# Kernel tuning notes

Measured on AMD Instinct MI355X. Metric: run time of the kernel, lower is better.

## Reference

```python
import jax, jax.numpy as jnp
import numpy as np

BS, F, C, H, W = 2, 8, 64, 128, 128
HEADS = 4

def build_edges(bs, f):
    rows, cols, ec = [], [], 0
    for b in range(bs):
        s = b * (2 * f + 2)
        v = list(range(s, s + f)); d = list(range(s + f, s + 2 * f))
        t = s + 2 * f; g = t + 1
        for grp in (v, d, v + d, v + d, v + d + [t], [t], [g]):
            rows += grp; cols += [ec] * len(grp); ec += 1
    return np.asarray(rows, np.int32), np.asarray(cols, np.int32), ec

ROW, COL, NUM_EDGES = build_edges(BS, F)

def conv2d_s2(x, w, b):  # Conv2d k3 s2 p1 + ReLU
    y = jax.lax.conv_general_dilated(x, w, (2, 2), [(1, 1), (1, 1)],
        dimension_numbers=('NCHW', 'OIHW', 'NCHW'))
    return jax.nn.relu(y + b[None, :, None, None])

def conv_t2(x, w, b):  # ConvTranspose2d k3 s2 p1 op1 + ReLU; w: (in,out,3,3)
    wt = jnp.flip(w, (2, 3)).transpose(1, 0, 2, 3)
    y = jax.lax.conv_general_dilated(x, wt, (1, 1), [(1, 2), (1, 2)],
        lhs_dilation=(2, 2), dimension_numbers=('NCHW', 'OIHW', 'NCHW'))
    return jax.nn.relu(y + b[None, :, None, None])

def layer_norm(x, eps=1e-5):  # affine params are default ones/zeros
    mu = x.mean(-1, keepdims=True)
    var = ((x - mu) ** 2).mean(-1, keepdims=True)
    return (x - mu) / jnp.sqrt(var + eps)

def group_norm(x, groups=32, eps=1e-5):
    n, c = x.shape
    xg = x.reshape(n, groups, c // groups)
    mu = xg.mean(-1, keepdims=True)
    var = ((xg - mu) ** 2).mean(-1, keepdims=True)
    return ((xg - mu) / jnp.sqrt(var + eps)).reshape(n, c)

def se_layer(x, w1, w2):  # squeeze over node dim 0
    y = jax.nn.sigmoid(jax.nn.relu(x.mean(0) @ w1.T) @ w2.T)
    return x * y

def hypergraph_conv(x, lin_w, att, edge_w, edge_attr, out_ch):
    # PyG HypergraphConv, use_attention=True, attention_mode='node', heads=4,
    # concat=False, bias=False, eval mode (dropout inactive)
    n = x.shape[0]
    xl = (x @ lin_w.T).reshape(n, HEADS, out_ch)
    ea = (edge_attr @ lin_w.T).reshape(-1, HEADS, out_ch)
    a = (jnp.concatenate([xl[ROW], ea[COL]], axis=-1) * att).sum(-1)  # (E, heads)
    a = jax.nn.leaky_relu(a, 0.2)
    a = jnp.exp(a - jax.ops.segment_max(a, COL, num_segments=NUM_EDGES)[COL])
    a = a / (jax.ops.segment_sum(a, COL, num_segments=NUM_EDGES)[COL] + 1e-16)
    D = jax.ops.segment_sum(edge_w[COL], ROW, num_segments=n)
    D = jnp.where(D > 0, 1.0 / D, 0.0)
    B = jax.ops.segment_sum(jnp.ones(ROW.shape[0], x.dtype), COL, num_segments=NUM_EDGES)
    B = jnp.where(B > 0, 1.0 / B, 0.0)
    e = jax.ops.segment_sum(B[COL][:, None, None] * a[:, :, None] * xl[ROW], COL, num_segments=NUM_EDGES)
    o = jax.ops.segment_sum(D[ROW][:, None, None] * a[:, :, None] * e[COL], ROW, num_segments=n)
    return o.mean(1)  # concat=False -> head mean

def setup_inputs() -> dict:
    key = jax.random.key(0)
    ks = jax.random.split(key, 32)
    def n(k, shape, s=1.0):
        return jax.random.normal(k, shape, jnp.float32) * s
    def u(k, shape):
        return jax.random.uniform(k, shape, jnp.float32)
    return {
        'vision_feat': n(ks[0], (BS, F, C, H, W)), 'vision_pos': n(ks[1], (BS, F, C, H, W), 0.1),
        'motion_feat': n(ks[2], (BS, F, C, H, W)), 'motion_pos': n(ks[3], (BS, F, C, H, W), 0.1),
        'text_feat': n(ks[4], (BS, C, 16)), 'text_pos': n(ks[5], (BS, C, 16), 0.1),
        'cv1_w': n(ks[6], (2 * C, C, 3, 3), 0.04), 'cv1_b': n(ks[7], (2 * C,), 0.01),
        'cv2_w': n(ks[8], (4 * C, 2 * C, 3, 3), 0.03), 'cv2_b': n(ks[9], (4 * C,), 0.01),
        'dc1_w': n(ks[10], (2 * C, C, 3, 3), 0.04), 'dc1_b': n(ks[11], (2 * C,), 0.01),
        'dc2_w': n(ks[12], (4 * C, 2 * C, 3, 3), 0.03), 'dc2_b': n(ks[13], (4 * C,), 0.01),
        'tc1_w': n(ks[14], (4 * C, 2 * C, 3, 3), 0.03), 'tc1_b': n(ks[15], (2 * C,), 0.01),
        'tc2_w': n(ks[16], (2 * C, C, 3, 3), 0.04), 'tc2_b': n(ks[17], (C,), 0.01),
        'lin1_w': n(ks[18], (HEADS * 8 * C, 4 * C), 0.06), 'att1': n(ks[19], (1, HEADS, 16 * C), 0.05),
        'lin2_w': n(ks[20], (HEADS * 4 * C, 8 * C), 0.04), 'att2': n(ks[21], (1, HEADS, 8 * C), 0.05),
        'ew1': u(ks[22], (2 * F * BS + 2,)), 'ew2': u(ks[23], (2 * F * BS + 2,)),
        'ea1': u(ks[24], (2 * F * BS + 2, 4 * C)), 'ea2': u(ks[25], (2 * F * BS + 2, 8 * C)),
        'se1_w1': n(ks[26], (8 * C // 16, 8 * C), 0.06), 'se1_w2': n(ks[27], (8 * C, 8 * C // 16), 0.15),
        'se2_w1': n(ks[28], (4 * C // 16, 4 * C), 0.08), 'se2_w2': n(ks[29], (4 * C, 4 * C // 16), 0.2),
    }

def reference(vision_feat, vision_pos, motion_feat, motion_pos, text_feat, text_pos,
              cv1_w, cv1_b, cv2_w, cv2_b, dc1_w, dc1_b, dc2_w, dc2_b,
              tc1_w, tc1_b, tc2_w, tc2_b, lin1_w, att1, lin2_w, att2,
              ew1, ew2, ea1, ea2, se1_w1, se1_w2, se2_w1, se2_w2):
    bs, f, c, h, w = vision_feat.shape
    # text_pool: AdaptiveMaxPool1d(4) on L=16 -> exact windows of 4; view(bs,-1)
    tn = (text_feat + text_pos).reshape(bs, c, 4, 4).max(-1).reshape(bs, 4 * c)
    v0 = (vision_feat + vision_pos).reshape(bs * f, c, h, w)
    v1 = conv2d_s2(v0, cv1_w, cv1_b)          # (bs*f, 2c, h/2, w/2)
    v2 = conv2d_s2(v1, cv2_w, cv2_b)          # (bs*f, 4c, h/4, w/4)
    vn = layer_norm(v2.max((2, 3)))           # AdaptiveMaxPool2d(1) + LayerNorm
    d0 = (motion_feat + motion_pos).reshape(bs * f, c, h, w)
    dn = layer_norm(conv2d_s2(conv2d_s2(d0, dc1_w, dc1_b), dc2_w, dc2_b).max((2, 3)))
    vb = vn.reshape(bs, f, 4 * c); db = dn.reshape(bs, f, 4 * c)
    obs = tn + (vb + db).mean(1)              # observer = mean(text+v+d) over frames
    x = jnp.concatenate([vb, db, tn[:, None], obs[:, None]], axis=1).reshape(bs * (2 * f + 2), 4 * c)
    x = se_layer(group_norm(jax.nn.relu(hypergraph_conv(x, lin1_w, att1, ew1, ea1, 8 * c))), se1_w1, se1_w2)
    x = se_layer(group_norm(jax.nn.relu(hypergraph_conv(x, lin2_w, att2, ew2, ea2, 4 * c))), se2_w1, se2_w2)
    xb = x.reshape(bs, 2 * f + 2, 4 * c)
    # obs_pool: AdaptiveMaxPool1d(c) on L=4c -> windows of 4
    observers = (tn + xb[:, -1]).reshape(bs, c, 4).max(-1)
    vg = xb[:, :f].reshape(bs * f, 4 * c)
    # bilinear upsample of 1x1 == broadcast; transconv doubles size so the
    # subsequent F.interpolate calls to (h/2,w/2) and (h,w) are identities
    vr = v2 + vg[:, :, None, None]
    vr = v1 + conv_t2(vr, tc1_w, tc1_b)
    vr = v0 + conv_t2(vr, tc2_w, tc2_b)
    return vr, observers
```

## Files before the change

### kernel.cpp

```cpp
#include <hip/hip_runtime.h>
#include <hip/hip_bf16.h>
#include <cstddef>
#include <cstdint>

#define DEV_INLINE __device__ __forceinline__
#define AS1 __attribute__((address_space(1)))
#define AS3 __attribute__((address_space(3)))

typedef __attribute__((ext_vector_type(8))) short short8;
typedef __attribute__((ext_vector_type(4))) float f32x4;
typedef __attribute__((ext_vector_type(2))) float f32x2;
typedef __attribute__((ext_vector_type(4))) unsigned short us4;

DEV_INLINE unsigned short f2bf(float f) {
  uint32_t u = __builtin_bit_cast(uint32_t, f);
  uint32_t r = (u + 0x7fffu + ((u >> 16) & 1u)) >> 16;
  return (unsigned short)r;
}
DEV_INLINE float bf2f(unsigned short u) {
  return __builtin_bit_cast(float, (uint32_t)u << 16);
}

DEV_INLINE void gl_lds16(const float* g, float* l) {
  __builtin_amdgcn_global_load_lds((AS1 void*)const_cast<float*>(g),
                                   (AS3 void*)l, 16, 0, 0);
}

__device__ __constant__ int c_cs[15] = {0,8,16,32,48,65,66,67,75,83,99,115,132,133,134};
__device__ __constant__ int c_row[134] = {
  0,1,2,3,4,5,6,7,
  8,9,10,11,12,13,14,15,
  0,1,2,3,4,5,6,7,8,9,10,11,12,13,14,15,
  0,1,2,3,4,5,6,7,8,9,10,11,12,13,14,15,
  0,1,2,3,4,5,6,7,8,9,10,11,12,13,14,15,16,
  16,
  17,
  18,19,20,21,22,23,24,25,
  26,27,28,29,30,31,32,33,
  18,19,20,21,22,23,24,25,26,27,28,29,30,31,32,33,
  18,19,20,21,22,23,24,25,26,27,28,29,30,31,32,33,
  18,19,20,21,22,23,24,25,26,27,28,29,30,31,32,33,34,
  34,
  35
};
__device__ __constant__ int c_col[134] = {
  0,0,0,0,0,0,0,0,
  1,1,1,1,1,1,1,1,
  2,2,2,2,2,2,2,2,2,2,2,2,2,2,2,2,
  3,3,3,3,3,3,3,3,3,3,3,3,3,3,3,3,
  4,4,4,4,4,4,4,4,4,4,4,4,4,4,4,4,4,
  5,
  6,
  7,7,7,7,7,7,7,7,
  8,8,8,8,8,8,8,8,
  9,9,9,9,9,9,9,9,9,9,9,9,9,9,9,9,
  10,10,10,10,10,10,10,10,10,10,10,10,10,10,10,10,
  11,11,11,11,11,11,11,11,11,11,11,11,11,11,11,11,11,
  12,
  13
};

__global__ __launch_bounds__(256) void k_prep(const float* __restrict__ a,
                                              const float* __restrict__ b,
                                              unsigned short* __restrict__ o) {
  __shared__ float sa[16 * 260];
  __shared__ float sb[16 * 260];
  int bid = blockIdx.x;
  int xb = bid & 1, y = (bid >> 1) & 127, n = bid >> 8;
  int t = threadIdx.x;
  int w = t >> 6, lane = t & 63;
  int ciq = lane >> 4;
  int xo = (lane & 15) * 4;
  const size_t base = ((size_t)n * 64) * 16384 + (size_t)y * 128 + xb * 64;
#pragma unroll
  for (int k = 0; k < 4; ++k) {
    int row = w * 16 + k * 4;
    const float* ga = a + base + (size_t)(row + ciq) * 16384 + xo;
    const float* gb = b + base + (size_t)(row + ciq) * 16384 + xo;
    gl_lds16(ga, &sa[(4 * w + k) * 260]);
    gl_lds16(gb, &sb[(4 * w + k) * 260]);
  }
  __syncthreads();
  auto rd = [](const float* s, int ci, int x) {
    return s[(ci >> 2) * 260 + (ci & 3) * 64 + x];
  };
  unsigned int* op = (unsigned int*)(o + (((size_t)n * 128 + y) * 128 + xb * 64) * 64);
#pragma unroll
  for (int it = 0; it < 2; ++it) {
    int i = t + it * 256;
    int x = i >> 3, cq = i & 7;
    uint4 v;
    unsigned int vv[4];
#pragma unroll
    for (int j = 0; j < 4; ++j) {
      int c2 = cq * 8 + j * 2;
      unsigned int lo = f2bf(rd(sa, c2, x) + rd(sb, c2, x));
      unsigned int hi = f2bf(rd(sa, c2 + 1, x) + rd(sb, c2 + 1, x));
      vv[j] = lo | (hi << 16);
    }
    v.x = vv[0]; v.y = vv[1]; v.z = vv[2]; v.w = vv[3];
    *reinterpret_cast<uint4*>(op + x * 32 + cq * 4) = v;
  }
}

__global__ void k_wtrans_all(const float* __restrict__ cv1w, const float* __restrict__ dc1w,
                             const float* __restrict__ cv2w, const float* __restrict__ dc2w,
                             const float* __restrict__ tc1w, const float* __restrict__ tc2w,
                             unsigned short* __restrict__ wtb) {
  int idx = blockIdx.x * 256 + threadIdx.x;
  const float* src; int off, lci, lco; bool tra;
  if (idx < 73728)        { src = cv1w; off = 0;       lci = 6; lco = 7; tra = false; }
  else if (idx < 147456)  { src = dc1w; off = 73728;   lci = 6; lco = 7; tra = false; }
  else if (idx < 442368)  { src = cv2w; off = 147456;  lci = 7; lco = 8; tra = false; }
  else if (idx < 737280)  { src = dc2w; off = 442368;  lci = 7; lco = 8; tra = false; }
  else if (idx < 1032192) { src = tc1w; off = 737280;  lci = 8; lco = 7; tra = true;  }
  else if (idx < 1105920) { src = tc2w; off = 1032192; lci = 7; lco = 6; tra = true;  }
  else return;
  int l = idx - off;
  int ci = l & ((1 << lci) - 1);
  int r = l >> lci;
  int co = r & ((1 << lco) - 1);
  int tap = r >> lco;
  size_t si = tra ? (((size_t)ci << lco) + co) * 9 + tap
                  : (((size_t)co << lci) + ci) * 9 + tap;
  wtb[idx] = f2bf(src[si]);
}

template<int CI, int CO, int HO, int WO, int ROUT>
__global__ __launch_bounds__(512, 3) void k_conv_mfma(
    const unsigned short* __restrict__ in,
    const unsigned short* __restrict__ wT,
    const float* __restrict__ bias,
    unsigned short* __restrict__ outn) {
  constexpr int HIN = HO * 2, WIN = WO * 2;
  constexpr int XHP = WO + 2;
  constexpr int R = 2 * ROUT + 1;
  constexpr int NPOS = R * 2 * XHP;
  constexpr int NCH = NPOS * 4;
  constexpr int NCS = CI / 32;
  constexpr int KIT = (NCH + 511) / 512;
  constexpr int CB = CO / 128;
  constexpr int OB = HO / ROUT;
  __shared__ short8 sIn[NPOS * 5];
  int bid = blockIdx.x;
  int cb = bid % CB; bid /= CB;
  int oyb = bid % OB; int n = bid / OB;
  int tid = threadIdx.x;
  int wid = tid >> 6, lane = tid & 63;
  int wm = wid >> 1, wn = wid & 1;
  int llo = lane & 15, lhi = lane >> 4;
  f32x4 acc[2][2] = {};
  const int iy0 = oyb * (2 * ROUT) - 1;
  short8 rv[KIT];
  auto loadr = [&](int cs) {
#pragma unroll
    for (int k = 0; k < KIT; ++k) {
      int i = tid + k * 512;
      short8 v = {};
      if (i < NCH) {
        int c = i & 3, q = i >> 2;
        int xh = q % XHP; int q2 = q / XHP;
        int p = q2 & 1, l = q2 >> 1;
        int x = 2 * xh + p - 1;
        int iy = iy0 + l;
        if (x >= 0 && x < WIN && iy >= 0 && iy < HIN)
          v = *reinterpret_cast<const short8*>(in + ((((size_t)n * HIN + iy) * WIN + x) * CI + cs * 32 + c * 8));
      }
      rv[k] = v;
    }
  };
  auto writes = [&]() {
#pragma unroll
    for (int k = 0; k < KIT; ++k) {
      int i = tid + k * 512;
      if (i < NCH) sIn[(i >> 2) * 5 + (i & 3)] = rv[k];
    }
  };
  loadr(0);
  for (int cs = 0; cs < NCS; ++cs) {
    writes();
    __syncthreads();
    if (cs + 1 < NCS) loadr(cs + 1);
    short8 afr9[9][2];
#pragma unroll
    for (int tap = 0; tap < 9; ++tap)
#pragma unroll
      for (int m = 0; m < 2; ++m) {
        int co = cb * 128 + wm * 32 + m * 16 + llo;
        afr9[tap][m] = *reinterpret_cast<const short8*>(wT + (((size_t)tap * CO + co) * CI + cs * 32 + lhi * 8));
      }
#pragma unroll
    for (int tap = 0; tap < 9; ++tap) {
      const int ky = tap / 3, kx = tap % 3;
      short8 bfr[2];
#pragma unroll
      for (int n2 = 0; n2 < 2; ++n2) {
        int pix = wn * 32 + n2 * 16 + llo;
        int oyl = (ROUT == 2) ? (pix >> 5) : 0;
        int ox = pix - oyl * WO;
        int lrow = 2 * oyl + ky;
        int pos = (lrow * 2 + (kx & 1)) * XHP + ox + (kx >> 1);
        bfr[n2] = sIn[pos * 5 + lhi];
      }
#pragma unroll
      for (int m = 0; m < 2; ++m)
#pragma unroll
        for (int n2 = 0; n2 < 2; ++n2)
          acc[m][n2] = __builtin_amdgcn_mfma_f32_16x16x32_bf16(afr9[tap][m], bfr[n2], acc[m][n2], 0, 0, 0);
    }
    __syncthreads();
  }
#pragma unroll
  for (int m = 0; m < 2; ++m) {
    int co0 = cb * 128 + wm * 32 + m * 16 + lhi * 4;
    f32x4 bv = *reinterpret_cast<const f32x4*>(bias + co0);
#pragma unroll
    for (int n2 = 0; n2 < 2; ++n2) {
      int pix = wn * 32 + n2 * 16 + llo;
      int oyl = (ROUT == 2) ? (pix >> 5) : 0;
      int ox = pix - oyl * WO;
      int oy = oyb * ROUT + oyl;
      us4 pk;
      pk[0] = f2bf(fmaxf(acc[m][n2][0] + bv[0], 0.f));
      pk[1] = f2bf(fmaxf(acc[m][n2][1] + bv[1], 0.f));
      pk[2] = f2bf(fmaxf(acc[m][n2][2] + bv[2], 0.f));
      pk[3] = f2bf(fmaxf(acc[m][n2][3] + bv[3], 0.f));
      *reinterpret_cast<us4*>(outn + ((((size_t)n * HO + oy) * WO + ox) * CO + co0)) = pk;
    }
  }
}

template<int CI, int CO, int Hi, int Wi, int QR, bool OBF, bool GADD>
__global__ __launch_bounds__(256, 3) void k_deconv_mfma(
    const unsigned short* __restrict__ in,
    const unsigned short* __restrict__ wT,
    const float* __restrict__ bias,
    const unsigned short* __restrict__ resn,
    const float* __restrict__ gsrc,
    unsigned short* __restrict__ outn,
    float* __restrict__ outc) {
  constexpr int QC = 64 / QR;
  constexpr int WP = Wi + 1;
  constexpr int NPOS = (QR + 1) * WP;
  constexpr int NCH = NPOS * 4;
  constexpr int NCS = CI / 32;
  constexpr int KIT = (NCH + 255) / 256;
  constexpr int CB = CO / 64;
  constexpr int OB = Hi / QR;
  constexpr int Ho = Hi * 2, Wo = Wi * 2;
  __shared__ short8 sIn[NPOS * 5];
  int bid = blockIdx.x;
  int cb = bid % CB; bid /= CB;
  int oyb = bid % OB; int n = bid / OB;
  int tid = threadIdx.x;
  int wid = tid >> 6, lane = tid & 63;
  int wm = wid >> 1, wn = wid & 1;
  int llo = lane & 15, lhi = lane >> 4;
  int qy0 = oyb * QR;
  const float* g = nullptr;
  if constexpr (GADD) g = gsrc + ((size_t)((n >> 3) * 18 + (n & 7))) * 256;
  f32x4 acc[4][2][2] = {};
  constexpr int tap_p[9] = {3,2,3,1,0,1,3,2,3};
  constexpr int tap_b[9] = {3,2,2,1,0,0,1,0,0};
  short8 rv[KIT];
  auto loadr = [&](int cs) {
#pragma unroll
    for (int k = 0; k < KIT; ++k) {
      int i = tid + k * 256;
      short8 v = {};
      if (i < NCH) {
        int c = i & 3, q = i >> 2;
        int x = q % WP, l = q / WP;
        int iy = qy0 + l;
        if (x < Wi && iy < Hi) {
          v = *reinterpret_cast<const short8*>(in + (((size_t)(n * Hi + iy) * Wi + x) * CI + cs * 32 + c * 8));
          if constexpr (GADD) {
#pragma unroll
            for (int j = 0; j < 8; ++j) {
              float fv = bf2f((unsigned short)v[j]) + g[cs * 32 + c * 8 + j];
              v[j] = (short)f2bf(fv);
            }
          }
        }
      }
      rv[k] = v;
    }
  };
  auto writes = [&]() {
#pragma unroll
    for (int k = 0; k < KIT; ++k) {
      int i = tid + k * 256;
      if (i < NCH) sIn[(i >> 2) * 5 + (i & 3)] = rv[k];
    }
  };
  loadr(0);
  for (int cs = 0; cs < NCS; ++cs) {
    writes();
    __syncthreads();
    if (cs + 1 < NCS) loadr(cs + 1);
    short8 bfr[2][4];
#pragma unroll
    for (int n2 = 0; n2 < 2; ++n2) {
      int pix = wn * 32 + n2 * 16 + llo;
      int qyl = pix / QC, qx = pix % QC;
#pragma unroll
      for (int bs = 0; bs < 4; ++bs) {
        int pos = (qyl + (bs >> 1)) * WP + qx + (bs & 1);
        bfr[n2][bs] = sIn[pos * 5 + lhi];
      }
    }
#pragma unroll
    for (int m = 0; m < 2; ++m) {
      short8 afr9[9];
#pragma unroll
      for (int tap = 0; tap < 9; ++tap) {
        int co = cb * 64 + wm * 32 + m * 16 + llo;
        afr9[tap] = *reinterpret_cast<const short8*>(wT + (((size_t)tap * CO + co) * CI + cs * 32 + lhi * 8));
      }
#pragma unroll
      for (int tap = 0; tap < 9; ++tap)
#pragma unroll
        for (int n2 = 0; n2 < 2; ++n2)
          acc[tap_p[tap]][m][n2] = __builtin_amdgcn_mfma_f32_16x16x32_bf16(
              afr9[tap], bfr[n2][tap_b[tap]], acc[tap_p[tap]][m][n2], 0, 0, 0);
    }
    __syncthreads();
  }
#pragma unroll
  for (int m = 0; m < 2; ++m) {
    int co0 = cb * 64 + wm * 32 + m * 16 + lhi * 4;
    f32x4 bv = *reinterpret_cast<const f32x4*>(bias + co0);
#pragma unroll
    for (int n2 = 0; n2 < 2; ++n2) {
      int pix = wn * 32 + n2 * 16 + llo;
      int qyl = pix / QC, qx = pix % QC;
      int qy = qy0 + qyl;
      if constexpr (OBF) {
#pragma unroll
        for (int p = 0; p < 4; ++p) {
          int oy = 2 * qy + (p >> 1);
          int ox = 2 * qx + (p & 1);
          size_t ad = ((size_t)(n * Ho + oy) * Wo + ox) * CO + co0;
          us4 r = *reinterpret_cast<const us4*>(resn + ad);
          us4 pk;
#pragma unroll
          for (int c = 0; c < 4; ++c)
            pk[c] = f2bf(bf2f(r[c]) + fmaxf(acc[p][m][n2][c] + bv[c], 0.f));
          *reinterpret_cast<us4*>(outn + ad) = pk;
        }
      } else {
        int qx2 = 2 * qx;
#pragma unroll
        for (int dy = 0; dy < 2; ++dy) {
          int oy = 2 * qy + dy;
          size_t rb = ((size_t)(n * Ho + oy) * Wo + qx2) * CO + co0;
          us4 r0 = *reinterpret_cast<const us4*>(resn + rb);
          us4 r1 = *reinterpret_cast<const us4*>(resn + rb + CO);
#pragma unroll
          for (int c = 0; c < 4; ++c) {
            f32x2 st;
            st[0] = bf2f(r0[c]) + fmaxf(acc[dy * 2][m][n2][c] + bv[c], 0.f);
            st[1] = bf2f(r1[c]) + fmaxf(acc[dy * 2 + 1][m][n2][c] + bv[c], 0.f);
            __builtin_nontemporal_store(st,
                reinterpret_cast<f32x2*>(outc + ((size_t)(n * CO + co0 + c) * Ho + oy) * Wo + qx2));
          }
        }
      }
    }
  }
}

__global__ __launch_bounds__(256) void k_max_part(const unsigned short* __restrict__ x,
                                                  float* __restrict__ pmax) {
  int n = blockIdx.x >> 3, pg = blockIdx.x & 7;
  int t = threadIdx.x;
  int c8 = t & 31;
  int ps = t >> 5;
  const unsigned short* base = x + (size_t)n * 262144 + (size_t)pg * 32768 + (size_t)c8 * 8;
  float m[8];
#pragma unroll
  for (int j = 0; j < 8; ++j) m[j] = -1e30f;
  for (int p = ps * 16; p < ps * 16 + 16; ++p) {
    short8 v = *reinterpret_cast<const short8*>(base + (size_t)p * 256);
#pragma unroll
    for (int j = 0; j < 8; ++j) m[j] = fmaxf(m[j], bf2f((unsigned short)v[j]));
  }
  __shared__ float sred[8][264];
#pragma unroll
  for (int j = 0; j < 8; ++j) sred[ps][c8 * 8 + j] = m[j];
  __syncthreads();
  float mm = sred[0][t];
#pragma unroll
  for (int g = 1; g < 8; ++g) mm = fmaxf(mm, sred[g][t]);
  pmax[((size_t)n * 8 + pg) * 256 + t] = mm;
}

__global__ __launch_bounds__(256) void k_ln(const float* __restrict__ pmax,
                                            float* __restrict__ out) {
  int n = blockIdx.x, ch = threadIdx.x;
  float m = -1e30f;
#pragma unroll
  for (int g = 0; g < 8; ++g)
    m = fmaxf(m, pmax[((size_t)n * 8 + g) * 256 + ch]);
  __shared__ float r1[256], r2[256];
  r1[ch] = m; __syncthreads();
  for (int s = 128; s > 0; s >>= 1) { if (ch < s) r1[ch] += r1[ch + s]; __syncthreads(); }
  float mu = r1[0] * (1.f / 256.f);
  float d = m - mu;
  r2[ch] = d * d; __syncthreads();
  for (int s = 128; s > 0; s >>= 1) { if (ch < s) r2[ch] += r2[ch + s]; __syncthreads(); }
  out[(size_t)n * 256 + ch] = d * rsqrtf(r2[0] * (1.f / 256.f) + 1e-5f);
}

__global__ void k_build_x(const float* __restrict__ tf, const float* __restrict__ tp,
                          const float* __restrict__ vn, const float* __restrict__ dn,
                          float* __restrict__ tn, float* __restrict__ x0) {
  int b = blockIdx.x, ch = threadIdx.x;
  int c4 = ch >> 2, j = ch & 3;
  const float* p = tf + ((size_t)b * 64 + c4) * 16 + j * 4;
  const float* q = tp + ((size_t)b * 64 + c4) * 16 + j * 4;
  float tv = p[0] + q[0];
  tv = fmaxf(tv, p[1] + q[1]);
  tv = fmaxf(tv, p[2] + q[2]);
  tv = fmaxf(tv, p[3] + q[3]);
  tn[(size_t)b * 256 + ch] = tv;
  float s = 0.f;
  for (int f = 0; f < 8; ++f) {
    float vv = vn[((size_t)b * 8 + f) * 256 + ch];
    float dd = dn[((size_t)b * 8 + f) * 256 + ch];
    s += vv + dd;
    x0[((size_t)b * 18 + f) * 256 + ch] = vv;
    x0[((size_t)b * 18 + 8 + f) * 256 + ch] = dd;
  }
  x0[((size_t)b * 18 + 16) * 256 + ch] = tv;
  x0[((size_t)b * 18 + 17) * 256 + ch] = tv + s * (1.f / 8.f);
}

__global__ __launch_bounds__(256) void k_gnn_lin(
    const float* __restrict__ x, const float* __restrict__ ea,
    const float* __restrict__ w, float* __restrict__ y, int K, int M) {
  int chunks = M >> 8;
  int r = blockIdx.x / chunks;
  int ob = (blockIdx.x % chunks) * 256 + threadIdx.x;
  const float* src = (r < 36) ? (x + (size_t)r * K) : (ea + (size_t)(r - 36) * K);
  __shared__ __align__(16) float sxr[512];
  for (int k = threadIdx.x; k < K; k += 256) sxr[k] = src[k];
  __syncthreads();
  const float4* w4 = reinterpret_cast<const float4*>(w + (size_t)ob * K);
  const float4* x4 = reinterpret_cast<const float4*>(sxr);
  float acc = 0.f;
  int k4 = K >> 2;
  for (int k = 0; k < k4; ++k) {
    float4 a = x4[k], b = w4[k];
    acc += a.x * b.x + a.y * b.y + a.z * b.z + a.w * b.w;
  }
  y[(size_t)r * M + ob] = acc;
}

template<int OC>
__global__ __launch_bounds__(256) void k_gnn_attsm(
    const float* __restrict__ y, const float* __restrict__ att,
    float* __restrict__ attw) {
  int t = threadIdx.x;
  __shared__ float sx_s[144], seb_s[60];
  __shared__ float a_s[536];
  if (t < 200) {
    int r = t >> 2, h = t & 3;
    const float4* row = reinterpret_cast<const float4*>(y + ((size_t)r * 4 + h) * OC);
    const float4* ar = reinterpret_cast<const float4*>(att + (size_t)h * 2 * OC + (r < 36 ? 0 : OC));
    float s = 0.f;
#pragma unroll 4
    for (int k = 0; k < OC / 4; ++k) {
      float4 a = row[k], b = ar[k];
      s += a.x * b.x + a.y * b.y + a.z * b.z + a.w * b.w;
    }
    if (r < 36) sx_s[r * 4 + h] = s; else seb_s[(r - 36) * 4 + h] = s;
  }
  __syncthreads();
  for (int idx = t; idx < 536; idx += 256) {
    int i = idx >> 2, h = idx & 3;
    float v = sx_s[c_row[i] * 4 + h] + seb_s[c_col[i] * 4 + h];
    a_s[idx] = (v > 0.f) ? v : 0.2f * v;
  }
  __syncthreads();
  if (t < 56) {
    int c = t >> 2, h = t & 3;
    int st = c_cs[c], en = c_cs[c + 1];
    float m = -1e30f;
    for (int i = st; i < en; ++i) m = fmaxf(m, a_s[i * 4 + h]);
    float s = 0.f;
    for (int i = st; i < en; ++i) { float e = __expf(a_s[i * 4 + h] - m); a_s[i * 4 + h] = e; s += e; }
    float inv = 1.f / (s + 1e-16f);
    for (int i = st; i < en; ++i) a_s[i * 4 + h] *= inv;
  }
  __syncthreads();
  for (int idx = t; idx < 536; idx += 256) attw[idx] = a_s[idx];
}

template<int OC>
__global__ __launch_bounds__(256) void k_edge_agg(
    const float* __restrict__ y, const float* __restrict__ attw,
    float* __restrict__ eb) {
  int idx = blockIdx.x * 256 + threadIdx.x;
  if (idx >= 14 * 4 * OC) return;
  int ch = idx % OC;
  int h = (idx / OC) & 3;
  int c = idx / (4 * OC);
  int st = c_cs[c], en = c_cs[c + 1];
  float s = 0.f;
  for (int i = st; i < en; ++i)
    s += attw[i * 4 + h] * y[(size_t)c_row[i] * (4 * OC) + h * OC + ch];
  eb[idx] = s * (1.f / (float)(en - st));
}

template<int OC>
__global__ __launch_bounds__(256) void k_node_agg(
    const float* __restrict__ attw, const float* __restrict__ eb,
    const float* __restrict__ ew, float* __restrict__ ho) {
  int idx = blockIdx.x * 256 + threadIdx.x;
  if (idx >= 36 * OC) return;
  int ch = idx % OC;
  int node = idx / OC;
  int b = node / 18, ln = node % 18;
  int ncols, cols[4], gis[4];
  if (ln < 16) {
    ncols = 4;
    cols[0] = b * 7 + (ln < 8 ? 0 : 1); gis[0] = b * 67 + ln;
    cols[1] = b * 7 + 2; gis[1] = b * 67 + 16 + ln;
    cols[2] = b * 7 + 3; gis[2] = b * 67 + 32 + ln;
    cols[3] = b * 7 + 4; gis[3] = b * 67 + 48 + ln;
  } else if (ln == 16) {
    ncols = 2;
    cols[0] = b * 7 + 4; gis[0] = b * 67 + 64;
    cols[1] = b * 7 + 5; gis[1] = b * 67 + 65;
    cols[2] = cols[3] = 0; gis[2] = gis[3] = 0;
  } else {
    ncols = 1;
    cols[0] = b * 7 + 6; gis[0] = b * 67 + 66;
    cols[1] = cols[2] = cols[3] = 0; gis[1] = gis[2] = gis[3] = 0;
  }
  float dsum = 0.f;
#pragma unroll
  for (int k = 0; k < 4; ++k) if (k < ncols) dsum += ew[cols[k]];
  float D = dsum > 0.f ? 1.f / dsum : 0.f;
  float s = 0.f;
#pragma unroll
  for (int k = 0; k < 4; ++k) {
    if (k < ncols) {
#pragma unroll
      for (int h = 0; h < 4; ++h)
        s += attw[gis[k] * 4 + h] * eb[((size_t)cols[k] * 4 + h) * OC + ch];
    }
  }
  ho[idx] = fmaxf(0.25f * D * s, 0.f);
}

template<int C, int Cr>
__global__ __launch_bounds__(512) void k_gn_se(
    const float* __restrict__ hin, const float* __restrict__ w1,
    const float* __restrict__ w2, float* __restrict__ x) {
  int t = threadIdx.x;
  constexpr int gs = C >> 5;
  for (int idx = t; idx < 36 * 32; idx += 512) {
    int node = idx >> 5, g = idx & 31;
    const float* p = hin + (size_t)node * C + g * gs;
    float s = 0.f, s2 = 0.f;
#pragma unroll
    for (int k = 0; k < gs; ++k) { float v = p[k]; s += v; s2 += v * v; }
    float mu = s * (1.f / gs);
    float var = s2 * (1.f / gs) - mu * mu;
    float inv = rsqrtf(fmaxf(var, 0.f) + 1e-5f);
    float* q = x + (size_t)node * C + g * gs;
#pragma unroll
    for (int k = 0; k < gs; ++k) q[k] = (p[k] - mu) * inv;
  }
  __threadfence_block();
  __syncthreads();
  __shared__ float smean[C];
  __shared__ float spart[Cr][17];
  __shared__ float shid[Cr];
  __shared__ float sscale[C];
  if (t < C) {
    float s = 0.f;
    for (int nn = 0; nn < 36; ++nn) s += x[(size_t)nn * C + t];
    smean[t] = s * (1.f / 36.f);
  }
  __syncthreads();
  if (t < Cr * 16) {
    int hid = t >> 4, sub = t & 15;
    constexpr int CH = C / 16;
    float s = 0.f;
#pragma unroll
    for (int k = 0; k < CH; ++k)
      s += w1[(size_t)hid * C + sub * CH + k] * smean[sub * CH + k];
    spart[hid][sub] = s;
  }
  __syncthreads();
  if (t < Cr) {
    float s = 0.f;
#pragma unroll
    for (int k = 0; k < 16; ++k) s += spart[t][k];
    shid[t] = fmaxf(s, 0.f);
  }
  __syncthreads();
  if (t < C) {
    float s = 0.f;
#pragma unroll
    for (int k = 0; k < Cr; ++k) s += w2[(size_t)t * Cr + k] * shid[k];
    sscale[t] = 1.f / (1.f + __expf(-s));
  }
  __syncthreads();
  for (int idx = t; idx < 36 * C; idx += 512) x[idx] *= sscale[idx % C];
}

__global__ void k_obs(const float* __restrict__ tn, const float* __restrict__ x2,
                      float* __restrict__ out) {
  int t = threadIdx.x;
  if (t >= 128) return;
  int b = t >> 6, ch = t & 63;
  const float* a = tn + (size_t)b * 256 + ch * 4;
  const float* c = x2 + ((size_t)b * 18 + 17) * 256 + ch * 4;
  float m = a[0] + c[0];
  m = fmaxf(m, a[1] + c[1]);
  m = fmaxf(m, a[2] + c[2]);
  m = fmaxf(m, a[3] + c[3]);
  out[b * 64 + ch] = m;
}

extern "C" void kernel_launch(void* const* d_in, const int* in_sizes, int n_in,
                              void* d_out, int out_size, void* d_ws, size_t ws_size,
                              hipStream_t stream) {
  (void)in_sizes; (void)n_in; (void)out_size; (void)ws_size;
  const float* vf    = (const float*)d_in[0];
  const float* vp    = (const float*)d_in[1];
  const float* mf    = (const float*)d_in[2];
  const float* mp    = (const float*)d_in[3];
  const float* tf    = (const float*)d_in[4];
  const float* tp    = (const float*)d_in[5];
  const float* cv1w  = (const float*)d_in[6];
  const float* cv1b  = (const float*)d_in[7];
  const float* cv2w  = (const float*)d_in[8];
  const float* cv2b  = (const float*)d_in[9];
  const float* dc1w  = (const float*)d_in[10];
  const float* dc1b  = (const float*)d_in[11];
  const float* dc2w  = (const float*)d_in[12];
  const float* dc2b  = (const float*)d_in[13];
  const float* tc1w  = (const float*)d_in[14];
  const float* tc1b  = (const float*)d_in[15];
  const float* tc2w  = (const float*)d_in[16];
  const float* tc2b  = (const float*)d_in[17];
  const float* lin1w = (const float*)d_in[18];
  const float* att1  = (const float*)d_in[19];
  const float* lin2w = (const float*)d_in[20];
  const float* att2  = (const float*)d_in[21];
  const float* ew1   = (const float*)d_in[22];
  const float* ew2   = (const float*)d_in[23];
  const float* ea1   = (const float*)d_in[24];
  const float* ea2   = (const float*)d_in[25];
  const float* se1w1 = (const float*)d_in[26];
  const float* se1w2 = (const float*)d_in[27];
  const float* se2w1 = (const float*)d_in[28];
  const float* se2w2 = (const float*)d_in[29];

  float* ws  = (float*)d_ws;
  float* out = (float*)d_out;

  unsigned short* p0n = (unsigned short*)(ws);
  unsigned short* q1n = (unsigned short*)(ws + 8388608);
  unsigned short* t1n = (unsigned short*)(ws + 12582912);
  unsigned short* v2n = (unsigned short*)(ws + 16777216);
  unsigned short* wtb = (unsigned short*)(ws + 18874368);
  float* sm   = ws + 19427328;
  float* tn   = sm;
  float* vn   = sm + 512;
  float* dn   = sm + 4608;
  float* x0   = sm + 8704;
  float* xl   = sm + 17920;
  float* eb   = sm + 120520;
  float* ho   = sm + 149192;
  float* x1   = sm + 167624;
  float* x2   = sm + 186056;
  float* attw = sm + 195272;
  float* pmax = sm + 195904;

  unsigned short* wTc1 = wtb;
  unsigned short* wTd1 = wtb + 73728;
  unsigned short* wTc2 = wtb + 147456;
  unsigned short* wTd2 = wtb + 442368;
  unsigned short* wTt1 = wtb + 737280;
  unsigned short* wTt2 = wtb + 1032192;

  k_wtrans_all<<<4320, 256, 0, stream>>>(cv1w, dc1w, cv2w, dc2w, tc1w, tc2w, wtb);

  k_prep<<<4096, 256, 0, stream>>>(mf, mp, p0n);
  k_conv_mfma<64, 128, 64, 64, 1><<<1024, 512, 0, stream>>>(p0n, wTd1, dc1b, q1n);
  k_conv_mfma<128, 256, 32, 32, 2><<<512, 512, 0, stream>>>(q1n, wTd2, dc2b, v2n);
  k_max_part<<<128, 256, 0, stream>>>(v2n, pmax);
  k_ln<<<16, 256, 0, stream>>>(pmax, dn);

  k_prep<<<4096, 256, 0, stream>>>(vf, vp, p0n);
  k_conv_mfma<64, 128, 64, 64, 1><<<1024, 512, 0, stream>>>(p0n, wTc1, cv1b, q1n);
  k_conv_mfma<128, 256, 32, 32, 2><<<512, 512, 0, stream>>>(q1n, wTc2, cv2b, v2n);
  k_max_part<<<128, 256, 0, stream>>>(v2n, pmax);
  k_ln<<<16, 256, 0, stream>>>(pmax, vn);

  k_build_x<<<2, 256, 0, stream>>>(tf, tp, vn, dn, tn, x0);

  k_gnn_lin<<<50 * 8, 256, 0, stream>>>(x0, ea1, lin1w, xl, 256, 2048);
  k_gnn_attsm<512><<<1, 256, 0, stream>>>(xl, att1, attw);
  k_edge_agg<512><<<112, 256, 0, stream>>>(xl, attw, eb);
  k_node_agg<512><<<72, 256, 0, stream>>>(attw, eb, ew1, ho);
  k_gn_se<512, 32><<<1, 512, 0, stream>>>(ho, se1w1, se1w2, x1);

  k_gnn_lin<<<50 * 4, 256, 0, stream>>>(x1, ea2, lin2w, xl, 512, 1024);
  k_gnn_attsm<256><<<1, 256, 0, stream>>>(xl, att2, attw);
  k_edge_agg<256><<<56, 256, 0, stream>>>(xl, attw, eb);
  k_node_agg<256><<<36, 256, 0, stream>>>(attw, eb, ew2, ho);
  k_gn_se<256, 16><<<1, 512, 0, stream>>>(ho, se2w1, se2w2, x2);

  k_obs<<<1, 128, 0, stream>>>(tn, x2, out + 16777216);

  k_deconv_mfma<256, 128, 32, 32, 2, true, true><<<512, 256, 0, stream>>>(
      v2n, wTt1, tc1b, q1n, x2, t1n, nullptr);
  k_deconv_mfma<128, 64, 64, 64, 1, false, false><<<1024, 256, 0, stream>>>(
      t1n, wTt2, tc2b, p0n, nullptr, nullptr, out);
}
```

Before: 480.6 us.

## Batch motion and visual encoder branches into single conv launches

The motion and visual conv encoder branches were run back to back, each with its own launches. They now run in shared launches: the conv kernels pick input, weights and bias per block from the batch index, and max-pool and layer norm run once over both branches. This doubles the grid of each launch to fill the GPU better and halves the launch count. k_prep is also reshaped to 512 threads per full row, reusing one LDS buffer for both input tensors. Workspace layout changes, and the output buffer is used as scratch for intermediates.

```diff
diff --git a/kernel.cpp b/kernel.cpp
--- a/kernel.cpp
+++ b/kernel.cpp
@@ -60,43 +60,53 @@
   13
 };
 
-__global__ __launch_bounds__(256) void k_prep(const float* __restrict__ a,
+__global__ __launch_bounds__(512) void k_prep(const float* __restrict__ a,
                                               const float* __restrict__ b,
                                               unsigned short* __restrict__ o) {
-  __shared__ float sa[16 * 260];
-  __shared__ float sb[16 * 260];
+  __shared__ float sbuf[32 * 260];
   int bid = blockIdx.x;
-  int xb = bid & 1, y = (bid >> 1) & 127, n = bid >> 8;
+  int y = bid & 127, n = bid >> 7;
   int t = threadIdx.x;
   int w = t >> 6, lane = t & 63;
-  int ciq = lane >> 4;
-  int xo = (lane & 15) * 4;
-  const size_t base = ((size_t)n * 64) * 16384 + (size_t)y * 128 + xb * 64;
+  int cio = lane >> 5;
+  int xg4 = (lane & 31) * 4;
+  const size_t base = ((size_t)n * 64) * 16384 + (size_t)y * 128;
 #pragma unroll
   for (int k = 0; k < 4; ++k) {
-    int row = w * 16 + k * 4;
-    const float* ga = a + base + (size_t)(row + ciq) * 16384 + xo;
-    const float* gb = b + base + (size_t)(row + ciq) * 16384 + xo;
-    gl_lds16(ga, &sa[(4 * w + k) * 260]);
-    gl_lds16(gb, &sb[(4 * w + k) * 260]);
-  }
-  __syncthreads();
-  auto rd = [](const float* s, int ci, int x) {
-    return s[(ci >> 2) * 260 + (ci & 3) * 64 + x];
+    int c = w * 4 + k;
+    gl_lds16(a + base + (size_t)(2 * c + cio) * 16384 + xg4, &sbuf[c * 260]);
+  }
+  __syncthreads();
+  auto rd = [&](int ci, int x) {
+    return sbuf[(ci >> 1) * 260 + (ci & 1) * 128 + x];
   };
-  unsigned int* op = (unsigned int*)(o + (((size_t)n * 128 + y) * 128 + xb * 64) * 64);
+  float av[2][8];
 #pragma unroll
   for (int it = 0; it < 2; ++it) {
-    int i = t + it * 256;
+    int i = t + it * 512;
+    int x = i >> 3, cq = i & 7;
+#pragma unroll
+    for (int j = 0; j < 8; ++j) av[it][j] = rd(cq * 8 + j, x);
+  }
+  __syncthreads();
+#pragma unroll
+  for (int k = 0; k < 4; ++k) {
+    int c = w * 4 + k;
+    gl_lds16(b + base + (size_t)(2 * c + cio) * 16384 + xg4, &sbuf[c * 260]);
+  }
+  __syncthreads();
+  unsigned int* op = (unsigned int*)(o + (((size_t)n * 128 + y) * 128) * 64);
+#pragma unroll
+  for (int it = 0; it < 2; ++it) {
+    int i = t + it * 512;
     int x = i >> 3, cq = i & 7;
     uint4 v;
     unsigned int vv[4];
 #pragma unroll
-    for (int j = 0; j < 4; ++j) {
-      int c2 = cq * 8 + j * 2;
-      unsigned int lo = f2bf(rd(sa, c2, x) + rd(sb, c2, x));
-      unsigned int hi = f2bf(rd(sa, c2 + 1, x) + rd(sb, c2 + 1, x));
-      vv[j] = lo | (hi << 16);
+    for (int jj = 0; jj < 4; ++jj) {
+      unsigned int lo = f2bf(av[it][2 * jj]     + rd(cq * 8 + 2 * jj, x));
+      unsigned int hi = f2bf(av[it][2 * jj + 1] + rd(cq * 8 + 2 * jj + 1, x));
+      vv[jj] = lo | (hi << 16);
     }
     v.x = vv[0]; v.y = vv[1]; v.z = vv[2]; v.w = vv[3];
     *reinterpret_cast<uint4*>(op + x * 32 + cq * 4) = v;
@@ -126,11 +136,11 @@
   wtb[idx] = f2bf(src[si]);
 }
 
-template<int CI, int CO, int HO, int WO, int ROUT>
-__global__ __launch_bounds__(512, 3) void k_conv_mfma(
-    const unsigned short* __restrict__ in,
-    const unsigned short* __restrict__ wT,
-    const float* __restrict__ bias,
+template<int CI, int CO, int HO, int WO, int ROUT, bool SPLIT_IN>
+__global__ __launch_bounds__(512, 3) void k_conv_mfma_b(
+    const unsigned short* __restrict__ in0, const unsigned short* __restrict__ in1,
+    const unsigned short* __restrict__ wT0, const unsigned short* __restrict__ wT1,
+    const float* __restrict__ b0, const float* __restrict__ b1,
     unsigned short* __restrict__ outn) {
   constexpr int HIN = HO * 2, WIN = WO * 2;
   constexpr int XHP = WO + 2;
@@ -145,6 +155,11 @@
   int bid = blockIdx.x;
   int cb = bid % CB; bid /= CB;
   int oyb = bid % OB; int n = bid / OB;
+  int br = n >> 4;
+  const unsigned short* in = SPLIT_IN ? (br ? in1 : in0) : in0;
+  const unsigned short* wT = br ? wT1 : wT0;
+  const float* bias = br ? b1 : b0;
+  int ni = SPLIT_IN ? (n & 15) : n;
   int tid = threadIdx.x;
   int wid = tid >> 6, lane = tid & 63;
   int wm = wid >> 1, wn = wid & 1;
@@ -164,7 +179,7 @@
         int x = 2 * xh + p - 1;
         int iy = iy0 + l;
         if (x >= 0 && x < WIN && iy >= 0 && iy < HIN)
-          v = *reinterpret_cast<const short8*>(in + ((((size_t)n * HIN + iy) * WIN + x) * CI + cs * 32 + c * 8));
+          v = *reinterpret_cast<const short8*>(in + ((((size_t)ni * HIN + iy) * WIN + x) * CI + cs * 32 + c * 8));
       }
       rv[k] = v;
     }
@@ -413,7 +428,7 @@
 }
 
 __global__ void k_build_x(const float* __restrict__ tf, const float* __restrict__ tp,
-                          const float* __restrict__ vn, const float* __restrict__ dn,
+                          const float* __restrict__ nb,
                           float* __restrict__ tn, float* __restrict__ x0) {
   int b = blockIdx.x, ch = threadIdx.x;
   int c4 = ch >> 2, j = ch & 3;
@@ -424,6 +439,8 @@
   tv = fmaxf(tv, p[2] + q[2]);
   tv = fmaxf(tv, p[3] + q[3]);
   tn[(size_t)b * 256 + ch] = tv;
+  const float* dn = nb;
+  const float* vn = nb + 16 * 256;
   float s = 0.f;
   for (int f = 0; f < 8; ++f) {
     float vv = vn[((size_t)b * 8 + f) * 256 + ch];
@@ -665,15 +682,13 @@
   float* ws  = (float*)d_ws;
   float* out = (float*)d_out;
 
-  unsigned short* p0n = (unsigned short*)(ws);
-  unsigned short* q1n = (unsigned short*)(ws + 8388608);
-  unsigned short* t1n = (unsigned short*)(ws + 12582912);
-  unsigned short* v2n = (unsigned short*)(ws + 16777216);
-  unsigned short* wtb = (unsigned short*)(ws + 18874368);
-  float* sm   = ws + 19427328;
+  unsigned short* p0nm = (unsigned short*)(ws);
+  unsigned short* p0nv = (unsigned short*)(ws + 8388608);
+  unsigned short* q1nb = (unsigned short*)(ws + 16777216);
+  unsigned short* wtb  = (unsigned short*)(ws + 25165824);
+  float* sm   = ws + 25718784;
   float* tn   = sm;
-  float* vn   = sm + 512;
-  float* dn   = sm + 4608;
+  float* nb   = sm + 512;
   float* x0   = sm + 8704;
   float* xl   = sm + 17920;
   float* eb   = sm + 120520;
@@ -683,6 +698,9 @@
   float* attw = sm + 195272;
   float* pmax = sm + 195904;
 
+  unsigned short* v2nb = (unsigned short*)d_out;
+  unsigned short* t1n = (unsigned short*)(ws);
+
   unsigned short* wTc1 = wtb;
   unsigned short* wTd1 = wtb + 73728;
   unsigned short* wTc2 = wtb + 147456;
@@ -692,19 +710,17 @@
 
   k_wtrans_all<<<4320, 256, 0, stream>>>(cv1w, dc1w, cv2w, dc2w, tc1w, tc2w, wtb);
 
-  k_prep<<<4096, 256, 0, stream>>>(mf, mp, p0n);
-  k_conv_mfma<64, 128, 64, 64, 1><<<1024, 512, 0, stream>>>(p0n, wTd1, dc1b, q1n);
-  k_conv_mfma<128, 256, 32, 32, 2><<<512, 512, 0, stream>>>(q1n, wTd2, dc2b, v2n);
-  k_max_part<<<128, 256, 0, stream>>>(v2n, pmax);
-  k_ln<<<16, 256, 0, stream>>>(pmax, dn);
-
-  k_prep<<<4096, 256, 0, stream>>>(vf, vp, p0n);
-  k_conv_mfma<64, 128, 64, 64, 1><<<1024, 512, 0, stream>>>(p0n, wTc1, cv1b, q1n);
-  k_conv_mfma<128, 256, 32, 32, 2><<<512, 512, 0, stream>>>(q1n, wTc2, cv2b, v2n);
-  k_max_part<<<128, 256, 0, stream>>>(v2n, pmax);
-  k_ln<<<16, 256, 0, stream>>>(pmax, vn);
-
-  k_build_x<<<2, 256, 0, stream>>>(tf, tp, vn, dn, tn, x0);
+  k_prep<<<2048, 512, 0, stream>>>(mf, mp, p0nm);
+  k_prep<<<2048, 512, 0, stream>>>(vf, vp, p0nv);
+
+  k_conv_mfma_b<64, 128, 64, 64, 1, true><<<2048, 512, 0, stream>>>(
+      p0nm, p0nv, wTd1, wTc1, dc1b, cv1b, q1nb);
+  k_conv_mfma_b<128, 256, 32, 32, 2, false><<<1024, 512, 0, stream>>>(
+      q1nb, nullptr, wTd2, wTc2, dc2b, cv2b, v2nb);
+  k_max_part<<<256, 256, 0, stream>>>(v2nb, pmax);
+  k_ln<<<32, 256, 0, stream>>>(pmax, nb);
+
+  k_build_x<<<2, 256, 0, stream>>>(tf, tp, nb, tn, x0);
 
   k_gnn_lin<<<50 * 8, 256, 0, stream>>>(x0, ea1, lin1w, xl, 256, 2048);
   k_gnn_attsm<512><<<1, 256, 0, stream>>>(xl, att1, attw);
@@ -720,8 +736,10 @@
 
   k_obs<<<1, 128, 0, stream>>>(tn, x2, out + 16777216);
 
+  unsigned short* v2nv = v2nb + 4194304;
+  unsigned short* q1nv = q1nb + 8388608;
   k_deconv_mfma<256, 128, 32, 32, 2, true, true><<<512, 256, 0, stream>>>(
-      v2n, wTt1, tc1b, q1n, x2, t1n, nullptr);
+      v2nv, wTt1, tc1b, q1nv, x2, t1n, nullptr);
   k_deconv_mfma<128, 64, 64, 64, 1, false, false><<<1024, 256, 0, stream>>>(
-      t1n, wTt2, tc2b, p0n, nullptr, nullptr, out);
-}
+      t1n, wTt2, tc2b, p0nv, nullptr, nullptr, out);
+}
```

Result: faster. 462.4 us, median of 2 (-3.8%).
